# Kernel tuning notes

Measured on AMD Instinct MI355X. Metric: run time of the kernel, lower is better.

## Reference

```python
import jax, jax.numpy as jnp
import numpy as np

B, C, T, V = 8, 64, 16, 207
H, WSZ = 8, 4
EPS = 1e-5


def setup_inputs() -> dict:
    key = jax.random.key(0)
    ks = jax.random.split(key, 16)
    def w(k, shape):
        return jax.random.normal(k, shape, jnp.float32) * 0.02
    inp = {"x": jax.random.normal(ks[0], (B, C, T, V), jnp.float32)}
    for i, s in enumerate("ab"):
        o = 1 + i * 4
        inp[f"qkv_w_{s}"] = w(ks[o], (C, 3 * C))
        inp[f"qkv_b_{s}"] = jnp.zeros((3 * C,), jnp.float32)
        inp[f"proj_w_{s}"] = w(ks[o + 1], (C, C))
        inp[f"proj_b_{s}"] = jnp.zeros((C,), jnp.float32)
        inp[f"ffn_w1_{s}"] = w(ks[o + 2], (C, 4 * C))
        inp[f"ffn_b1_{s}"] = jnp.zeros((4 * C,), jnp.float32)
        inp[f"ffn_w2_{s}"] = w(ks[o + 3], (4 * C, C))
        inp[f"ffn_b2_{s}"] = jnp.zeros((C,), jnp.float32)
        inp[f"ln_{s}1_g"] = jnp.ones((C, T, V), jnp.float32)
        inp[f"ln_{s}1_b"] = jnp.zeros((C, T, V), jnp.float32)
        inp[f"ln_{s}2_g"] = jnp.ones((C, T, V), jnp.float32)
        inp[f"ln_{s}2_b"] = jnp.zeros((C, T, V), jnp.float32)
    inp["n_head"] = H
    inp["window_size"] = WSZ
    return inp


def _layer_norm(x, g, b):
    # LayerNorm over (C, T, V) dims of [B, C, T, V]
    mu = jnp.mean(x, axis=(1, 2, 3), keepdims=True)
    var = jnp.var(x, axis=(1, 2, 3), keepdims=True)
    return (x - mu) / jnp.sqrt(var + EPS) * g + b


def _window_att(x, wqkv, bqkv, wo, bo, n_head, wsz):
    # Joint spatio-temporal attention within windows of `wsz` timesteps.
    b_, c_, t_, v_ = x.shape
    nw = t_ // wsz
    dh = c_ // n_head
    # [B,C,T,V] -> [B,T,V,C] -> [B,nW, wsz*V, C]
    xt = jnp.transpose(x, (0, 2, 3, 1)).reshape(b_, nw, wsz * v_, c_)
    qkv = xt @ wqkv + bqkv  # [B,nW,N,3C]
    q, k, v = jnp.split(qkv, 3, axis=-1)
    def heads(t):
        return t.reshape(b_, nw, -1, n_head, dh).transpose(0, 1, 3, 2, 4)  # [B,nW,H,N,dh]
    q, k, v = heads(q), heads(k), heads(v)
    scale = 1.0 / jnp.sqrt(jnp.asarray(dh, jnp.float32))
    att = jax.nn.softmax(jnp.einsum('bwhnd,bwhmd->bwhnm', q, k) * scale, axis=-1)
    out = jnp.einsum('bwhnm,bwhmd->bwhnd', att, v)
    out = out.transpose(0, 1, 3, 2, 4).reshape(b_, nw, wsz * v_, c_) @ wo + bo
    return out.reshape(b_, t_, v_, c_).transpose(0, 3, 1, 2)


def _ffn(x, w1, b1, w2, b2):
    h = jax.nn.relu(jnp.einsum('bctv,cd->bdtv', x, w1) + b1[None, :, None, None])
    return jnp.einsum('bdtv,dc->bctv', h, w2) + b2[None, :, None, None]


def _block(x, wqkv, bqkv, wo, bo, w1, b1, w2, b2, g1, be1, g2, be2, n_head, wsz):
    x = _window_att(x, wqkv, bqkv, wo, bo, n_head, wsz) + x
    x = _layer_norm(x, g1, be1)
    x = _ffn(x, w1, b1, w2, b2) + x
    x = _layer_norm(x, g2, be2)
    # cyclic shift along time by shift_pixel = wsz // 2
    return jnp.roll(x, -(wsz // 2), axis=2)


def reference(x, qkv_w_a, qkv_b_a, proj_w_a, proj_b_a, ffn_w1_a, ffn_b1_a, ffn_w2_a, ffn_b2_a,
              ln_a1_g, ln_a1_b, ln_a2_g, ln_a2_b,
              qkv_w_b, qkv_b_b, proj_w_b, proj_b_b, ffn_w1_b, ffn_b1_b, ffn_w2_b, ffn_b2_b,
              ln_b1_g, ln_b1_b, ln_b2_g, ln_b2_b, n_head, window_size):
    x = _block(x, qkv_w_a, qkv_b_a, proj_w_a, proj_b_a, ffn_w1_a, ffn_b1_a, ffn_w2_a, ffn_b2_a,
               ln_a1_g, ln_a1_b, ln_a2_g, ln_a2_b, n_head, window_size)
    x = _block(x, qkv_w_b, qkv_b_b, proj_w_b, proj_b_b, ffn_w1_b, ffn_b1_b, ffn_w2_b, ffn_b2_b,
               ln_b1_g, ln_b1_b, ln_b2_g, ln_b2_b, n_head, window_size)
    return x
```

## Files before the change

kernel.cpp:

```cpp
#include <hip/hip_runtime.h>
#include <hip/hip_bf16.h>

#define Bb  8
#define Cc  64
#define Tt  16
#define Vv  207
#define Hh  8
#define DH  8
#define NW  4
#define WSZ 4
#define Nn  (WSZ*Vv)
#define NP  832
#define TV  (Tt*Vv)
#define CTV (Cc*Tt*Vv)
#define S   (Bb*CTV)
#define NBWH (Bb*NW*Hh)
#define EPSF 1e-5f
#define QSCALE 0.51006971401146f
#define FRAG_BWH (52*64*4)
#define LAYER_WSZ 49152

typedef __attribute__((ext_vector_type(4))) short bf16x4;
typedef __attribute__((ext_vector_type(4))) float f32x4;
typedef __attribute__((ext_vector_type(2))) unsigned int u32x2;
typedef __attribute__((ext_vector_type(4))) unsigned int u32x4;

static __device__ __forceinline__ short f2bf(float f) {
    union { float f; unsigned u; } v; v.f = f;
    unsigned r = (v.u + 0x7FFFu + ((v.u >> 16) & 1u)) >> 16;
    return (short)r;
}

static __device__ __forceinline__ bf16x4 pack4(float a, float b, float c, float d) {
    unsigned ua = __builtin_bit_cast(unsigned, a) + 0x8000u;
    unsigned ub = __builtin_bit_cast(unsigned, b) + 0x8000u;
    unsigned uc = __builtin_bit_cast(unsigned, c) + 0x8000u;
    unsigned ud = __builtin_bit_cast(unsigned, d) + 0x8000u;
    u32x2 t;
    t[0] = (ua >> 16) | (ub & 0xFFFF0000u);
    t[1] = (uc >> 16) | (ud & 0xFFFF0000u);
    return __builtin_bit_cast(bf16x4, t);
}

__global__ void prep_kernel(const float* __restrict__ qa, const float* __restrict__ pa,
                            const float* __restrict__ w1a, const float* __restrict__ w2a,
                            const float* __restrict__ qbw, const float* __restrict__ pbw,
                            const float* __restrict__ w1b, const float* __restrict__ w2b,
                            short* __restrict__ wf, float* __restrict__ stats,
                            short* __restrict__ qf, short* __restrict__ kf,
                            short* __restrict__ vf) {
    int i0 = blockIdx.x*256 + threadIdx.x;
    if (i0 < 64) stats[i0] = 0.f;
    for (int i = i0; i < 24576; i += 416*256) {
        int l = i / 12288; int f = i % 12288;
        const float* qw = l ? qbw : qa;
        const float* pw = l ? pbw : pa;
        const float* w1 = l ? w1b : w1a;
        const float* w2 = l ? w2b : w2a;
        short* dst = wf + l*LAYER_WSZ;
        bf16x4 out;
        if (f < 3072) {
            int s = f; int nt = s>>8; int kc = (s>>6)&3; int ln = s&63;
            int li = ln&15; int q = ln>>4;
            #pragma unroll
            for (int j = 0; j < 4; ++j) out[j] = f2bf(qw[(kc*16+q*4+j)*192 + nt*16+li]);
            *((bf16x4*)&dst[s*4]) = out;
        } else if (f < 4096) {
            int s = f-3072; int nt = s>>8; int kc = (s>>6)&3; int ln = s&63;
            int li = ln&15; int q = ln>>4;
            #pragma unroll
            for (int j = 0; j < 4; ++j) out[j] = f2bf(pw[(kc*16+q*4+j)*64 + nt*16+li]);
            *((bf16x4*)&dst[12288 + s*4]) = out;
        } else if (f < 8192) {
            int s = f-4096; int nt = s>>8; int kc = (s>>6)&3; int ln = s&63;
            int li = ln&15; int q = ln>>4;
            #pragma unroll
            for (int j = 0; j < 4; ++j) out[j] = f2bf(w1[(kc*16+q*4+j)*256 + nt*16+li]);
            *((bf16x4*)&dst[16384 + s*4]) = out;
        } else {
            int s = f-8192; int nt = s>>8; int ct = (s>>6)&3; int ln = s&63;
            int li = ln&15; int q = ln>>4;
            #pragma unroll
            for (int j = 0; j < 4; ++j) out[j] = f2bf(w2[(nt*16+q*4+j)*64 + ct*16+li]);
            *((bf16x4*)&dst[32768 + s*4]) = out;
        }
    }
    for (int i = i0; i < NBWH*1664; i += 416*256) {
        int bwh = i / 1664; int rest = i % 1664;
        int nt = rest >> 5; int u = rest & 31;
        size_t base = (size_t)bwh*FRAG_BWH + nt*256;
        *((u32x2*)&qf[base + (32+u)*4]) = (u32x2){0u,0u};
        *((u32x2*)&kf[base + (32+u)*4]) = (u32x2){0u,0u};
        int vlane = (u>>3)*16 + 8 + (u&7);
        short v = ((u&7) == 0) ? (short)0x3F80 : (short)0;
        bf16x4 vv4 = {v,v,v,v};
        *((bf16x4*)&vf[base + vlane*4]) = vv4;
    }
}

__global__ __launch_bounds__(256) void qkv_kernel(const float* __restrict__ src,
        const float* __restrict__ st, const float* __restrict__ g, const float* __restrict__ be,
        const short* __restrict__ wfq, const float* __restrict__ bias,
        short* __restrict__ qf, short* __restrict__ kf, short* __restrict__ vf) {
    __shared__ short wqs[12288];
    __shared__ float bqs[192];
    __shared__ short os[64*196];
    int tid = threadIdx.x;
    int b = blockIdx.x / 52;
    int r0 = (blockIdx.x % 52) * 64;
    const float* xb = src + (size_t)b*CTV;
    {
        const u32x2* wsrc = (const u32x2*)wfq;
        u32x2* wdst = (u32x2*)wqs;
        for (int s = tid; s < 3072; s += 256) wdst[s] = wsrc[s];
    }
    if (tid < 192) bqs[tid] = bias[tid];
    __syncthreads();

    int lane = tid & 63; int wv = tid >> 6;
    int l15 = lane & 15; int quad = lane >> 4;
    int r = r0 + wv*16 + l15;
    int rc = (r < TV) ? r : TV-1;
    int t = rc / Vv; int vv = rc - t*Vv;
    float mean = 0.f, rstd = 0.f; int off;
    if (st) {
        mean = st[b*2] * (1.0f/CTV);
        float var = st[b*2+1] * (1.0f/CTV) - mean*mean;
        rstd = rsqrtf(var + EPSF);
        off = ((t+2)&15)*Vv + vv;
    } else off = rc;

    bf16x4 xf[4];
    #pragma unroll
    for (int kc = 0; kc < 4; ++kc) {
        #pragma unroll
        for (int j = 0; j < 4; ++j) {
            int idx = (kc*16 + quad*4 + j)*TV + off;
            float xv = xb[idx];
            if (st) xv = (xv - mean)*rstd*g[idx] + be[idx];
            xf[kc][j] = f2bf(xv);
        }
    }

    f32x4 accv[12];
    #pragma unroll
    for (int nt = 0; nt < 12; ++nt) {
        float4 bb = *((const float4*)&bqs[nt*16 + quad*4]);
        f32x4 acc = {bb.x, bb.y, bb.z, bb.w};
        #pragma unroll
        for (int kc = 0; kc < 4; ++kc) {
            bf16x4 wf2 = *((const bf16x4*)&wqs[((nt*4 + kc)*64 + lane)*4]);
            acc = __builtin_amdgcn_mfma_f32_16x16x16bf16_1k(wf2, xf[kc], acc, 0, 0, 0);
        }
        accv[nt] = acc;
    }

    int pos = wv*16 + l15;
    #pragma unroll
    for (int nt = 0; nt < 12; ++nt) {
        f32x4 a = accv[nt];
        bf16x4 pk = (nt < 4) ? pack4(a[0]*QSCALE, a[1]*QSCALE, a[2]*QSCALE, a[3]*QSCALE)
                             : pack4(a[0], a[1], a[2], a[3]);
        *((bf16x4*)&os[pos*196 + nt*16 + quad*4]) = pk;
    }
    __syncthreads();

    int pp = tid & 63;
    int rr = r0 + pp;
    bool pv = rr < TV;
    int rrc = pv ? rr : TV-1;
    int t4 = rrc / Vv; int vv4 = rrc - t4*Vv;
    int n2 = (t4 & 3)*Vv + vv4;
    int nt2 = n2 >> 4; int l15n = n2 & 15;
    int quadn = (n2 & 15) >> 2; int jn = n2 & 3;
    int wbase = (b*NW + (t4 >> 2))*Hh;
    if (pv) {
        #pragma unroll
        for (int i = 0; i < 2; ++i) {
            int h = i*4 + wv;
            size_t fb = ((size_t)(wbase+h)*52 + nt2)*256;
            bf16x4 q0 = *((const bf16x4*)&os[pp*196 + h*8]);
            bf16x4 q1 = *((const bf16x4*)&os[pp*196 + h*8 + 4]);
            *((bf16x4*)&qf[fb + l15n*4])        = q0;
            *((bf16x4*)&qf[fb + (16 + l15n)*4]) = q1;
            bf16x4 k0 = *((const bf16x4*)&os[pp*196 + 64 + h*8]);
            bf16x4 k1 = *((const bf16x4*)&os[pp*196 + 64 + h*8 + 4]);
            *((bf16x4*)&kf[fb + l15n*4])        = k0;
            *((bf16x4*)&kf[fb + (16 + l15n)*4]) = k1;
        }
        #pragma unroll
        for (int i = 0; i < 16; ++i) {
            int hd = i*4 + wv;
            int h = hd >> 3; int d = hd & 7;
            vf[(((size_t)(wbase+h)*52 + nt2)*64 + quadn*16 + d)*4 + jn]
                = os[pp*196 + 128 + hd];
        }
    }
}

__global__ __launch_bounds__(1024) void attn_kernel(const short* __restrict__ qf,
        const short* __restrict__ kf, const short* __restrict__ vf,
        short* __restrict__ att) {
    __shared__ short ks2[FRAG_BWH];
    __shared__ short vs2[FRAG_BWH];
    int bwh = blockIdx.x;
    int tid = threadIdx.x;
    int lane = tid & 63;
    int wv = tid >> 6;
    int quad = lane >> 4;
    int l15 = lane & 15;

    {
        const u32x4* kg = (const u32x4*)(kf + (size_t)bwh*FRAG_BWH);
        const u32x4* vg = (const u32x4*)(vf + (size_t)bwh*FRAG_BWH);
        u32x4* kd = (u32x4*)ks2; u32x4* vd = (u32x4*)vs2;
        for (int idx = tid; idx < 1664; idx += 1024) { kd[idx] = kg[idx]; vd[idx] = vg[idx]; }
    }
    __syncthreads();

    int nm = (wv < 4) ? 4 : 3;
    const short* qbase = qf + (size_t)bwh*FRAG_BWH;
    bf16x4 aq[4];
    f32x4 oacc[4];
    #pragma unroll
    for (int i = 0; i < 4; ++i) {
        aq[i] = (bf16x4){0,0,0,0};
        oacc[i] = (f32x4){0.f,0.f,0.f,0.f};
        if (i < nm)
            aq[i] = *(const bf16x4*)(qbase + ((wv + 16*i)*256 + lane*4));
    }

    for (int nt = 0; nt < 52; ++nt) {
        bf16x4 ak = *(const bf16x4*)&ks2[nt*256 + lane*4];
        bf16x4 av = *(const bf16x4*)&vs2[nt*256 + lane*4];
        bool mask = (nt == 51) && (quad == 3);
        #pragma unroll
        for (int i = 0; i < 4; ++i) {
            if (i < nm) {
                f32x4 s = __builtin_amdgcn_mfma_f32_16x16x16bf16_1k(
                              ak, aq[i], (f32x4){0.f,0.f,0.f,0.f}, 0, 0, 0);
                bf16x4 pb = pack4(__builtin_amdgcn_exp2f(s[0]), __builtin_amdgcn_exp2f(s[1]),
                                  __builtin_amdgcn_exp2f(s[2]), __builtin_amdgcn_exp2f(s[3]));
                if (mask) pb = (bf16x4){0,0,0,0};
                oacc[i] = __builtin_amdgcn_mfma_f32_16x16x16bf16_1k(av, pb, oacc[i], 0, 0, 0);
            }
        }
    }
    int h = bwh & 7; int bw = bwh >> 3;
    #pragma unroll
    for (int i = 0; i < 4; ++i) {
        if (i < nm) {
            float ls = __shfl(oacc[i][0], 32 + l15, 64);
            float inv = 1.f / ls;
            int m = (wv + 16*i)*16 + l15;
            if (quad < 2 && m < Nn) {
                bf16x4 ov = pack4(oacc[i][0]*inv, oacc[i][1]*inv,
                                  oacc[i][2]*inv, oacc[i][3]*inv);
                *((bf16x4*)&att[((size_t)bw*Nn + m)*Cc + h*DH + quad*4]) = ov;
            }
        }
    }
}

__global__ __launch_bounds__(256) void proj_kernel(const short* __restrict__ att,
        const short* __restrict__ wfp, const float* __restrict__ bo,
        const float* __restrict__ resid,
        const float* __restrict__ st, const float* __restrict__ g, const float* __restrict__ be,
        float* __restrict__ out, float* __restrict__ stats) {
    __shared__ short wos[4096];
    __shared__ float bos[64];
    __shared__ float r1[256], r2[256];
    int tid = threadIdx.x;
    int b = blockIdx.x / 52;
    int r0 = (blockIdx.x % 52) * 64;
    const float* xb = resid + (size_t)b*CTV;
    {
        const u32x2* wsrc = (const u32x2*)wfp;
        u32x2* wdst = (u32x2*)wos;
        for (int s = tid; s < 1024; s += 256) wdst[s] = wsrc[s];
    }
    if (tid < 64) bos[tid] = bo[tid];
    __syncthreads();

    int lane = tid & 63; int wv = tid >> 6;
    int l15 = lane & 15; int quad = lane >> 4;
    int r = r0 + wv*16 + l15;
    bool valid = r < TV;
    int rc = valid ? r : TV-1;
    int t = rc / Vv; int vv = rc - t*Vv;
    int n = (t & 3)*Vv + vv;
    int bw = b*NW + (t >> 2);
    const short* arow = att + ((size_t)bw*Nn + n)*Cc;
    bf16x4 af[4];
    #pragma unroll
    for (int kc = 0; kc < 4; ++kc)
        af[kc] = *((const bf16x4*)&arow[kc*16 + quad*4]);

    f32x4 acc[4];
    #pragma unroll
    for (int nt = 0; nt < 4; ++nt) {
        float4 bb = *((const float4*)&bos[nt*16 + quad*4]);
        acc[nt] = (f32x4){bb.x, bb.y, bb.z, bb.w};
        #pragma unroll
        for (int kc = 0; kc < 4; ++kc) {
            bf16x4 wf2 = *((const bf16x4*)&wos[((nt*4 + kc)*64 + lane)*4]);
            acc[nt] = __builtin_amdgcn_mfma_f32_16x16x16bf16_1k(wf2, af[kc], acc[nt], 0, 0, 0);
        }
    }
    float mean = 0.f, rstd = 0.f; int off;
    if (st) {
        mean = st[b*2] * (1.0f/CTV);
        float var = st[b*2+1] * (1.0f/CTV) - mean*mean;
        rstd = rsqrtf(var + EPSF);
        off = ((t+2)&15)*Vv + vv;
    } else off = rc;
    float s1 = 0.f, s2 = 0.f;
    if (valid) {
        #pragma unroll
        for (int nt = 0; nt < 4; ++nt) {
            #pragma unroll
            for (int j = 0; j < 4; ++j) {
                int c_out = nt*16 + quad*4 + j;
                int ridx = c_out*TV + off;
                float xv = xb[ridx];
                if (st) xv = (xv - mean)*rstd*g[ridx] + be[ridx];
                float val = acc[nt][j] + xv;
                out[(size_t)b*CTV + (size_t)c_out*TV + r] = val;
                s1 += val; s2 += val*val;
            }
        }
    }
    r1[tid] = s1; r2[tid] = s2;
    __syncthreads();
    for (int o = 128; o > 0; o >>= 1) {
        if (tid < o) { r1[tid] += r1[tid+o]; r2[tid] += r2[tid+o]; }
        __syncthreads();
    }
    if (tid == 0) { atomicAdd(&stats[b*2], r1[0]); atomicAdd(&stats[b*2+1], r2[0]); }
}

__global__ void ln_apply_kernel(const float* __restrict__ x,
                                const float* __restrict__ g,
                                const float* __restrict__ be,
                                const float* __restrict__ stats,
                                float* __restrict__ out,
                                int shift) {
    int idx = blockIdx.x*256 + threadIdx.x;
    if (idx >= S) return;
    int b = idx / CTV; int r = idx % CTV;
    int c = r / TV; int q2 = r % TV; int t = q2 / Vv; int vv = q2 % Vv;
    float mean = stats[b*2] * (1.0f/CTV);
    float var  = stats[b*2+1] * (1.0f/CTV) - mean*mean;
    float rstd = rsqrtf(var + EPSF);
    float val = (x[idx]-mean)*rstd*g[r] + be[r];
    int tout = (t - shift + Tt) % Tt;
    size_t oidx = ((size_t)(b*Cc + c)*Tt + tout)*Vv + vv;
    out[oidx] = val;
}

__global__ __launch_bounds__(256) void ffn_kernel(const float* __restrict__ xin,
        const float* __restrict__ st, const float* __restrict__ g, const float* __restrict__ be,
        const short* __restrict__ wf1, const float* __restrict__ b1,
        const short* __restrict__ wf2g, const float* __restrict__ b2,
        float* __restrict__ out, float* __restrict__ stats) {
    __shared__ short w1s[16384];
    __shared__ short w2s[16384];
    __shared__ short xsf[4096];
    __shared__ float b1s[256];
    __shared__ float b2s[64];
    __shared__ float r1s[256], r2s[256];
    int tid = threadIdx.x;
    int b = blockIdx.x / 52;
    int r0 = (blockIdx.x % 52) * 64;
    const float* xb = xin + (size_t)b*CTV;
    float mean = st[b*2] * (1.0f/CTV);
    float var  = st[b*2+1] * (1.0f/CTV) - mean*mean;
    float rstd = rsqrtf(var + EPSF);

    {
        const u32x2* s1p = (const u32x2*)wf1;
        const u32x2* s2p = (const u32x2*)wf2g;
        u32x2* d1 = (u32x2*)w1s; u32x2* d2 = (u32x2*)w2s;
        for (int s = tid; s < 4096; s += 256) { d1[s] = s1p[s]; d2[s] = s2p[s]; }
    }
    for (int s2 = tid; s2 < 1024; s2 += 256) {
        int wv2 = s2 >> 8; int kc = (s2 >> 6) & 3; int ln = s2 & 63;
        int l15 = ln & 15; int quad = ln >> 4;
        int r = r0 + wv2*16 + l15; if (r >= TV) r = TV-1;
        bf16x4 f;
        #pragma unroll
        for (int j = 0; j < 4; ++j) {
            int idx = (kc*16 + quad*4 + j)*TV + r;
            f[j] = f2bf((xb[idx] - mean)*rstd*g[idx] + be[idx]);
        }
        *((bf16x4*)&xsf[s2*4]) = f;
    }
    b1s[tid] = b1[tid];
    if (tid < 64) b2s[tid] = b2[tid];
    __syncthreads();

    int lane = tid & 63; int wv = tid >> 6;
    int l15 = lane & 15; int quad = lane >> 4;
    bf16x4 xf[4];
    #pragma unroll
    for (int kc = 0; kc < 4; ++kc)
        xf[kc] = *((const bf16x4*)&xsf[((wv*4 + kc)*64 + lane)*4]);

    f32x4 oacc[4];
    #pragma unroll
    for (int ct = 0; ct < 4; ++ct) oacc[ct] = (f32x4){0.f,0.f,0.f,0.f};

    for (int nt = 0; nt < 16; ++nt) {
        float4 bb = *((const float4*)&b1s[nt*16 + quad*4]);
        f32x4 acc = {bb.x, bb.y, bb.z, bb.w};
        #pragma unroll
        for (int kc = 0; kc < 4; ++kc) {
            bf16x4 wfv = *((const bf16x4*)&w1s[((nt*4 + kc)*64 + lane)*4]);
            acc = __builtin_amdgcn_mfma_f32_16x16x16bf16_1k(wfv, xf[kc], acc, 0, 0, 0);
        }
        bf16x4 pf = pack4(fmaxf(acc[0], 0.f), fmaxf(acc[1], 0.f),
                          fmaxf(acc[2], 0.f), fmaxf(acc[3], 0.f));
        #pragma unroll
        for (int ct = 0; ct < 4; ++ct) {
            bf16x4 wfv2 = *((const bf16x4*)&w2s[((nt*4 + ct)*64 + lane)*4]);
            oacc[ct] = __builtin_amdgcn_mfma_f32_16x16x16bf16_1k(wfv2, pf, oacc[ct], 0, 0, 0);
        }
    }
    int r = r0 + wv*16 + l15;
    float s1 = 0.f, s2v = 0.f;
    if (r < TV) {
        #pragma unroll
        for (int ct = 0; ct < 4; ++ct) {
            #pragma unroll
            for (int j = 0; j < 4; ++j) {
                int c_out = ct*16 + quad*4 + j;
                int idx = c_out*TV + r;
                float xv = (xb[idx] - mean)*rstd*g[idx] + be[idx];
                float val = oacc[ct][j] + b2s[c_out] + xv;
                out[(size_t)b*CTV + idx] = val;
                s1 += val; s2v += val*val;
            }
        }
    }
    r1s[tid] = s1; r2s[tid] = s2v;
    __syncthreads();
    for (int o = 128; o > 0; o >>= 1) {
        if (tid < o) { r1s[tid] += r1s[tid+o]; r2s[tid] += r2s[tid+o]; }
        __syncthreads();
    }
    if (tid == 0) { atomicAdd(&stats[b*2], r1s[0]); atomicAdd(&stats[b*2+1], r2s[0]); }
}

extern "C" void kernel_launch(void* const* d_in, const int* in_sizes, int n_in,
                              void* d_out, int out_size, void* d_ws, size_t ws_size,
                              hipStream_t stream) {
    const float* xin = (const float*)d_in[0];

    float* bufA  = (float*)d_ws;
    float* bufB  = bufA + S;
    float* stats = bufB + S;
    short* qf    = (short*)(stats + 64);
    short* kf    = qf + (size_t)NBWH*FRAG_BWH;
    short* vf    = kf + (size_t)NBWH*FRAG_BWH;
    short* att   = vf + (size_t)NBWH*FRAG_BWH;
    short* wf    = att + (size_t)32*Nn*64;

    const float* A0  = (const float*)d_in[1];
    const float* A1  = (const float*)d_in[2];
    const float* A2  = (const float*)d_in[3];
    const float* A3  = (const float*)d_in[4];
    const float* A4  = (const float*)d_in[5];
    const float* A5  = (const float*)d_in[6];
    const float* A6  = (const float*)d_in[7];
    const float* A7  = (const float*)d_in[8];
    const float* A8  = (const float*)d_in[9];
    const float* A9  = (const float*)d_in[10];
    const float* A10 = (const float*)d_in[11];
    const float* A11 = (const float*)d_in[12];
    const float* B0  = (const float*)d_in[13];
    const float* B1  = (const float*)d_in[14];
    const float* B2  = (const float*)d_in[15];
    const float* B3  = (const float*)d_in[16];
    const float* B4  = (const float*)d_in[17];
    const float* B5  = (const float*)d_in[18];
    const float* B6  = (const float*)d_in[19];
    const float* B7  = (const float*)d_in[20];
    const float* B8  = (const float*)d_in[21];
    const float* B9  = (const float*)d_in[22];
    const float* B10 = (const float*)d_in[23];
    const float* B11 = (const float*)d_in[24];

    float* st1a = stats + 0;
    float* st2a = stats + 16;
    float* st1b = stats + 32;
    float* st2b = stats + 48;

    short* wfA = wf;
    short* wfB = wf + LAYER_WSZ;

    prep_kernel<<<416, 256, 0, stream>>>(A0, A2, A4, A6, B0, B2, B4, B6,
                                         wf, stats, qf, kf, vf);

    qkv_kernel<<<Bb*52, 256, 0, stream>>>(xin, nullptr, nullptr, nullptr,
                                          wfA, A1, qf, kf, vf);
    attn_kernel<<<NBWH, 1024, 0, stream>>>(qf, kf, vf, att);
    proj_kernel<<<Bb*52, 256, 0, stream>>>(att, wfA + 12288, A3, xin,
                                           nullptr, nullptr, nullptr, bufB, st1a);
    ffn_kernel<<<Bb*52, 256, 0, stream>>>(bufB, st1a, A8, A9,
                                          wfA + 16384, A5, wfA + 32768, A7, bufB, st2a);
    qkv_kernel<<<Bb*52, 256, 0, stream>>>(bufB, st2a, A10, A11,
                                          wfB, B1, qf, kf, vf);
    attn_kernel<<<NBWH, 1024, 0, stream>>>(qf, kf, vf, att);
    proj_kernel<<<Bb*52, 256, 0, stream>>>(att, wfB + 12288, B3, bufB,
                                           st2a, A10, A11, bufA, st1b);
    ffn_kernel<<<Bb*52, 256, 0, stream>>>(bufA, st1b, B8, B9,
                                          wfB + 16384, B5, wfB + 32768, B7, bufA, st2b);
    ln_apply_kernel<<<(S+255)/256, 256, 0, stream>>>(bufA, B10, B11, st2b, (float*)d_out, WSZ/2);
}
```

Measured before the change: 295.4 us.

## Fuse all stages into one cooperative persistent kernel with grid syncs

Replaces ten separate kernel launches with one cooperative mega-kernel of 512 blocks that runs each stage in turn, separated by grid-wide barriers, with the stages sharing one union of shared-memory layouts. The weight-prep kernel is removed and each block now converts fp32 weights to bf16 MFMA fragments itself when it loads them. Attention is split into two blocks of 256 threads per (batch, window, head) instead of one block of 1024. The aim is to cut launch overhead and inter-kernel gaps. In exchange, every block repeats the weight conversion, grid syncs have their own cost, and blocks 416 to 511 sit idle in most stages.

Measured after the change: 773.6 us. 2.62x slower.

```diff
diff --git a/kernel.cpp b/kernel.cpp
--- a/kernel.cpp
+++ b/kernel.cpp
@@ -1,5 +1,8 @@
 #include <hip/hip_runtime.h>
 #include <hip/hip_bf16.h>
+#include <hip/hip_cooperative_groups.h>
+
+namespace cg = cooperative_groups;
 
 #define Bb  8
 #define Cc  64
@@ -10,7 +13,6 @@
 #define NW  4
 #define WSZ 4
 #define Nn  (WSZ*Vv)
-#define NP  832
 #define TV  (Tt*Vv)
 #define CTV (Cc*Tt*Vv)
 #define S   (Bb*CTV)
@@ -18,7 +20,10 @@
 #define EPSF 1e-5f
 #define QSCALE 0.51006971401146f
 #define FRAG_BWH (52*64*4)
-#define LAYER_WSZ 49152
+
+#define GRID    512
+#define ACTIVE  416
+#define GSTRIDE (GRID*256)
 
 typedef __attribute__((ext_vector_type(4))) short bf16x4;
 typedef __attribute__((ext_vector_type(4))) float f32x4;
@@ -42,50 +47,19 @@
     return __builtin_bit_cast(bf16x4, t);
 }
 
-__global__ void prep_kernel(const float* __restrict__ qa, const float* __restrict__ pa,
-                            const float* __restrict__ w1a, const float* __restrict__ w2a,
-                            const float* __restrict__ qbw, const float* __restrict__ pbw,
-                            const float* __restrict__ w1b, const float* __restrict__ w2b,
-                            short* __restrict__ wf, float* __restrict__ stats,
-                            short* __restrict__ qf, short* __restrict__ kf,
-                            short* __restrict__ vf) {
-    int i0 = blockIdx.x*256 + threadIdx.x;
-    if (i0 < 64) stats[i0] = 0.f;
-    for (int i = i0; i < 24576; i += 416*256) {
-        int l = i / 12288; int f = i % 12288;
-        const float* qw = l ? qbw : qa;
-        const float* pw = l ? pbw : pa;
-        const float* w1 = l ? w1b : w1a;
-        const float* w2 = l ? w2b : w2a;
-        short* dst = wf + l*LAYER_WSZ;
-        bf16x4 out;
-        if (f < 3072) {
-            int s = f; int nt = s>>8; int kc = (s>>6)&3; int ln = s&63;
-            int li = ln&15; int q = ln>>4;
-            #pragma unroll
-            for (int j = 0; j < 4; ++j) out[j] = f2bf(qw[(kc*16+q*4+j)*192 + nt*16+li]);
-            *((bf16x4*)&dst[s*4]) = out;
-        } else if (f < 4096) {
-            int s = f-3072; int nt = s>>8; int kc = (s>>6)&3; int ln = s&63;
-            int li = ln&15; int q = ln>>4;
-            #pragma unroll
-            for (int j = 0; j < 4; ++j) out[j] = f2bf(pw[(kc*16+q*4+j)*64 + nt*16+li]);
-            *((bf16x4*)&dst[12288 + s*4]) = out;
-        } else if (f < 8192) {
-            int s = f-4096; int nt = s>>8; int kc = (s>>6)&3; int ln = s&63;
-            int li = ln&15; int q = ln>>4;
-            #pragma unroll
-            for (int j = 0; j < 4; ++j) out[j] = f2bf(w1[(kc*16+q*4+j)*256 + nt*16+li]);
-            *((bf16x4*)&dst[16384 + s*4]) = out;
-        } else {
-            int s = f-8192; int nt = s>>8; int ct = (s>>6)&3; int ln = s&63;
-            int li = ln&15; int q = ln>>4;
-            #pragma unroll
-            for (int j = 0; j < 4; ++j) out[j] = f2bf(w2[(nt*16+q*4+j)*64 + ct*16+li]);
-            *((bf16x4*)&dst[32768 + s*4]) = out;
-        }
-    }
-    for (int i = i0; i < NBWH*1664; i += 416*256) {
+struct SmQkv { short wqs[12288]; float bqs[192]; short os[64*196]; };
+struct SmAttn { short ks2[FRAG_BWH]; short vs2[FRAG_BWH]; };
+struct SmProj { short wos[4096]; float bos[64]; float r1[256]; float r2[256]; };
+struct SmFfn { short w1s[16384]; short w2s[16384]; short xsf[4096];
+               float b1s[256]; float b2s[64]; float r1s[256]; float r2s[256]; };
+
+static_assert(sizeof(SmQkv) <= sizeof(SmFfn), "");
+static_assert(sizeof(SmAttn) <= sizeof(SmFfn), "");
+static_assert(sizeof(SmProj) <= sizeof(SmFfn), "");
+
+static __device__ void pad_stage(short* __restrict__ qf, short* __restrict__ kf,
+                                 short* __restrict__ vf, int bid, int tid) {
+    for (int i = bid*256 + tid; i < NBWH*1664; i += GSTRIDE) {
         int bwh = i / 1664; int rest = i % 1664;
         int nt = rest >> 5; int u = rest & 31;
         size_t base = (size_t)bwh*FRAG_BWH + nt*256;
@@ -98,23 +72,23 @@
     }
 }
 
-__global__ __launch_bounds__(256) void qkv_kernel(const float* __restrict__ src,
+static __device__ void qkv_stage(const float* __restrict__ src,
         const float* __restrict__ st, const float* __restrict__ g, const float* __restrict__ be,
-        const short* __restrict__ wfq, const float* __restrict__ bias,
-        short* __restrict__ qf, short* __restrict__ kf, short* __restrict__ vf) {
-    __shared__ short wqs[12288];
-    __shared__ float bqs[192];
-    __shared__ short os[64*196];
-    int tid = threadIdx.x;
-    int b = blockIdx.x / 52;
-    int r0 = (blockIdx.x % 52) * 64;
+        const float* __restrict__ qw, const float* __restrict__ bias,
+        short* __restrict__ qf, short* __restrict__ kf, short* __restrict__ vf,
+        int bid, int tid, SmQkv& sm) {
+    int b = bid / 52;
+    int r0 = (bid % 52) * 64;
     const float* xb = src + (size_t)b*CTV;
-    {
-        const u32x2* wsrc = (const u32x2*)wfq;
-        u32x2* wdst = (u32x2*)wqs;
-        for (int s = tid; s < 3072; s += 256) wdst[s] = wsrc[s];
-    }
-    if (tid < 192) bqs[tid] = bias[tid];
+    for (int fs = tid; fs < 3072; fs += 256) {
+        int nt = fs >> 8; int kc = (fs >> 6) & 3; int ln = fs & 63;
+        int li = ln & 15; int q = ln >> 4;
+        bf16x4 o;
+        #pragma unroll
+        for (int j = 0; j < 4; ++j) o[j] = f2bf(qw[(kc*16 + q*4 + j)*192 + nt*16 + li]);
+        *((bf16x4*)&sm.wqs[fs*4]) = o;
+    }
+    if (tid < 192) sm.bqs[tid] = bias[tid];
     __syncthreads();
 
     int lane = tid & 63; int wv = tid >> 6;
@@ -145,11 +119,11 @@
     f32x4 accv[12];
     #pragma unroll
     for (int nt = 0; nt < 12; ++nt) {
-        float4 bb = *((const float4*)&bqs[nt*16 + quad*4]);
+        float4 bb = *((const float4*)&sm.bqs[nt*16 + quad*4]);
         f32x4 acc = {bb.x, bb.y, bb.z, bb.w};
         #pragma unroll
         for (int kc = 0; kc < 4; ++kc) {
-            bf16x4 wf2 = *((const bf16x4*)&wqs[((nt*4 + kc)*64 + lane)*4]);
+            bf16x4 wf2 = *((const bf16x4*)&sm.wqs[((nt*4 + kc)*64 + lane)*4]);
             acc = __builtin_amdgcn_mfma_f32_16x16x16bf16_1k(wf2, xf[kc], acc, 0, 0, 0);
         }
         accv[nt] = acc;
@@ -161,7 +135,7 @@
         f32x4 a = accv[nt];
         bf16x4 pk = (nt < 4) ? pack4(a[0]*QSCALE, a[1]*QSCALE, a[2]*QSCALE, a[3]*QSCALE)
                              : pack4(a[0], a[1], a[2], a[3]);
-        *((bf16x4*)&os[pos*196 + nt*16 + quad*4]) = pk;
+        *((bf16x4*)&sm.os[pos*196 + nt*16 + quad*4]) = pk;
     }
     __syncthreads();
 
@@ -179,12 +153,12 @@
         for (int i = 0; i < 2; ++i) {
             int h = i*4 + wv;
             size_t fb = ((size_t)(wbase+h)*52 + nt2)*256;
-            bf16x4 q0 = *((const bf16x4*)&os[pp*196 + h*8]);
-            bf16x4 q1 = *((const bf16x4*)&os[pp*196 + h*8 + 4]);
+            bf16x4 q0 = *((const bf16x4*)&sm.os[pp*196 + h*8]);
+            bf16x4 q1 = *((const bf16x4*)&sm.os[pp*196 + h*8 + 4]);
             *((bf16x4*)&qf[fb + l15n*4])        = q0;
             *((bf16x4*)&qf[fb + (16 + l15n)*4]) = q1;
-            bf16x4 k0 = *((const bf16x4*)&os[pp*196 + 64 + h*8]);
-            bf16x4 k1 = *((const bf16x4*)&os[pp*196 + 64 + h*8 + 4]);
+            bf16x4 k0 = *((const bf16x4*)&sm.os[pp*196 + 64 + h*8]);
+            bf16x4 k1 = *((const bf16x4*)&sm.os[pp*196 + 64 + h*8 + 4]);
             *((bf16x4*)&kf[fb + l15n*4])        = k0;
             *((bf16x4*)&kf[fb + (16 + l15n)*4]) = k1;
         }
@@ -193,50 +167,46 @@
             int hd = i*4 + wv;
             int h = hd >> 3; int d = hd & 7;
             vf[(((size_t)(wbase+h)*52 + nt2)*64 + quadn*16 + d)*4 + jn]
-                = os[pp*196 + 128 + hd];
-        }
-    }
-}
-
-__global__ __launch_bounds__(1024) void attn_kernel(const short* __restrict__ qf,
-        const short* __restrict__ kf, const short* __restrict__ vf,
-        short* __restrict__ att) {
-    __shared__ short ks2[FRAG_BWH];
-    __shared__ short vs2[FRAG_BWH];
-    int bwh = blockIdx.x;
-    int tid = threadIdx.x;
-    int lane = tid & 63;
-    int wv = tid >> 6;
-    int quad = lane >> 4;
-    int l15 = lane & 15;
-
+                = sm.os[pp*196 + 128 + hd];
+        }
+    }
+}
+
+static __device__ void attn_stage(const short* __restrict__ qf, const short* __restrict__ kf,
+        const short* __restrict__ vf, short* __restrict__ att,
+        int bid, int tid, SmAttn& sm) {
+    int bwh = bid >> 1;
+    int t0 = (bid & 1) * 26;
     {
         const u32x4* kg = (const u32x4*)(kf + (size_t)bwh*FRAG_BWH);
         const u32x4* vg = (const u32x4*)(vf + (size_t)bwh*FRAG_BWH);
-        u32x4* kd = (u32x4*)ks2; u32x4* vd = (u32x4*)vs2;
-        for (int idx = tid; idx < 1664; idx += 1024) { kd[idx] = kg[idx]; vd[idx] = vg[idx]; }
-    }
-    __syncthreads();
-
-    int nm = (wv < 4) ? 4 : 3;
+        u32x4* kd = (u32x4*)sm.ks2; u32x4* vd = (u32x4*)sm.vs2;
+        for (int idx = tid; idx < 1664; idx += 256) { kd[idx] = kg[idx]; vd[idx] = vg[idx]; }
+    }
+    __syncthreads();
+
+    int lane = tid & 63; int wv = tid >> 6;
+    int quad = lane >> 4; int l15 = lane & 15;
+    int ni = (wv < 2) ? 7 : 6;
     const short* qbase = qf + (size_t)bwh*FRAG_BWH;
-    bf16x4 aq[4];
-    f32x4 oacc[4];
-    #pragma unroll
-    for (int i = 0; i < 4; ++i) {
+    bf16x4 aq[7];
+    f32x4 oacc[7];
+    #pragma unroll
+    for (int i = 0; i < 7; ++i) {
         aq[i] = (bf16x4){0,0,0,0};
         oacc[i] = (f32x4){0.f,0.f,0.f,0.f};
-        if (i < nm)
-            aq[i] = *(const bf16x4*)(qbase + ((wv + 16*i)*256 + lane*4));
-    }
-
+        if (i < ni)
+            aq[i] = *(const bf16x4*)(qbase + (size_t)(t0 + wv + 4*i)*256 + lane*4);
+    }
+
+    #pragma unroll 1
     for (int nt = 0; nt < 52; ++nt) {
-        bf16x4 ak = *(const bf16x4*)&ks2[nt*256 + lane*4];
-        bf16x4 av = *(const bf16x4*)&vs2[nt*256 + lane*4];
+        bf16x4 ak = *(const bf16x4*)&sm.ks2[nt*256 + lane*4];
+        bf16x4 av = *(const bf16x4*)&sm.vs2[nt*256 + lane*4];
         bool mask = (nt == 51) && (quad == 3);
         #pragma unroll
-        for (int i = 0; i < 4; ++i) {
-            if (i < nm) {
+        for (int i = 0; i < 7; ++i) {
+            if (i < ni) {
                 f32x4 s = __builtin_amdgcn_mfma_f32_16x16x16bf16_1k(
                               ak, aq[i], (f32x4){0.f,0.f,0.f,0.f}, 0, 0, 0);
                 bf16x4 pb = pack4(__builtin_amdgcn_exp2f(s[0]), __builtin_amdgcn_exp2f(s[1]),
@@ -248,11 +218,11 @@
     }
     int h = bwh & 7; int bw = bwh >> 3;
     #pragma unroll
-    for (int i = 0; i < 4; ++i) {
-        if (i < nm) {
+    for (int i = 0; i < 7; ++i) {
+        if (i < ni) {
             float ls = __shfl(oacc[i][0], 32 + l15, 64);
             float inv = 1.f / ls;
-            int m = (wv + 16*i)*16 + l15;
+            int m = (t0 + wv + 4*i)*16 + l15;
             if (quad < 2 && m < Nn) {
                 bf16x4 ov = pack4(oacc[i][0]*inv, oacc[i][1]*inv,
                                   oacc[i][2]*inv, oacc[i][3]*inv);
@@ -262,24 +232,24 @@
     }
 }
 
-__global__ __launch_bounds__(256) void proj_kernel(const short* __restrict__ att,
-        const short* __restrict__ wfp, const float* __restrict__ bo,
+static __device__ void proj_stage(const short* __restrict__ att,
+        const float* __restrict__ pw, const float* __restrict__ bo,
         const float* __restrict__ resid,
         const float* __restrict__ st, const float* __restrict__ g, const float* __restrict__ be,
-        float* __restrict__ out, float* __restrict__ stats) {
-    __shared__ short wos[4096];
-    __shared__ float bos[64];
-    __shared__ float r1[256], r2[256];
-    int tid = threadIdx.x;
-    int b = blockIdx.x / 52;
-    int r0 = (blockIdx.x % 52) * 64;
+        float* __restrict__ out, float* __restrict__ stats,
+        int bid, int tid, SmProj& sm) {
+    int b = bid / 52;
+    int r0 = (bid % 52) * 64;
     const float* xb = resid + (size_t)b*CTV;
-    {
-        const u32x2* wsrc = (const u32x2*)wfp;
-        u32x2* wdst = (u32x2*)wos;
-        for (int s = tid; s < 1024; s += 256) wdst[s] = wsrc[s];
-    }
-    if (tid < 64) bos[tid] = bo[tid];
+    for (int fs = tid; fs < 1024; fs += 256) {
+        int nt = fs >> 8; int kc = (fs >> 6) & 3; int ln = fs & 63;
+        int li = ln & 15; int q = ln >> 4;
+        bf16x4 o;
+        #pragma unroll
+        for (int j = 0; j < 4; ++j) o[j] = f2bf(pw[(kc*16 + q*4 + j)*64 + nt*16 + li]);
+        *((bf16x4*)&sm.wos[fs*4]) = o;
+    }
+    if (tid < 64) sm.bos[tid] = bo[tid];
     __syncthreads();
 
     int lane = tid & 63; int wv = tid >> 6;
@@ -299,11 +269,11 @@
     f32x4 acc[4];
     #pragma unroll
     for (int nt = 0; nt < 4; ++nt) {
-        float4 bb = *((const float4*)&bos[nt*16 + quad*4]);
+        float4 bb = *((const float4*)&sm.bos[nt*16 + quad*4]);
         acc[nt] = (f32x4){bb.x, bb.y, bb.z, bb.w};
         #pragma unroll
         for (int kc = 0; kc < 4; ++kc) {
-            bf16x4 wf2 = *((const bf16x4*)&wos[((nt*4 + kc)*64 + lane)*4]);
+            bf16x4 wf2 = *((const bf16x4*)&sm.wos[((nt*4 + kc)*64 + lane)*4]);
             acc[nt] = __builtin_amdgcn_mfma_f32_16x16x16bf16_1k(wf2, af[kc], acc[nt], 0, 0, 0);
         }
     }
@@ -330,58 +300,39 @@
             }
         }
     }
-    r1[tid] = s1; r2[tid] = s2;
+    sm.r1[tid] = s1; sm.r2[tid] = s2;
     __syncthreads();
     for (int o = 128; o > 0; o >>= 1) {
-        if (tid < o) { r1[tid] += r1[tid+o]; r2[tid] += r2[tid+o]; }
+        if (tid < o) { sm.r1[tid] += sm.r1[tid+o]; sm.r2[tid] += sm.r2[tid+o]; }
         __syncthreads();
     }
-    if (tid == 0) { atomicAdd(&stats[b*2], r1[0]); atomicAdd(&stats[b*2+1], r2[0]); }
-}
-
-__global__ void ln_apply_kernel(const float* __restrict__ x,
-                                const float* __restrict__ g,
-                                const float* __restrict__ be,
-                                const float* __restrict__ stats,
-                                float* __restrict__ out,
-                                int shift) {
-    int idx = blockIdx.x*256 + threadIdx.x;
-    if (idx >= S) return;
-    int b = idx / CTV; int r = idx % CTV;
-    int c = r / TV; int q2 = r % TV; int t = q2 / Vv; int vv = q2 % Vv;
-    float mean = stats[b*2] * (1.0f/CTV);
-    float var  = stats[b*2+1] * (1.0f/CTV) - mean*mean;
-    float rstd = rsqrtf(var + EPSF);
-    float val = (x[idx]-mean)*rstd*g[r] + be[r];
-    int tout = (t - shift + Tt) % Tt;
-    size_t oidx = ((size_t)(b*Cc + c)*Tt + tout)*Vv + vv;
-    out[oidx] = val;
-}
-
-__global__ __launch_bounds__(256) void ffn_kernel(const float* __restrict__ xin,
+    if (tid == 0) { atomicAdd(&stats[b*2], sm.r1[0]); atomicAdd(&stats[b*2+1], sm.r2[0]); }
+}
+
+static __device__ void ffn_stage(const float* __restrict__ xin,
         const float* __restrict__ st, const float* __restrict__ g, const float* __restrict__ be,
-        const short* __restrict__ wf1, const float* __restrict__ b1,
-        const short* __restrict__ wf2g, const float* __restrict__ b2,
-        float* __restrict__ out, float* __restrict__ stats) {
-    __shared__ short w1s[16384];
-    __shared__ short w2s[16384];
-    __shared__ short xsf[4096];
-    __shared__ float b1s[256];
-    __shared__ float b2s[64];
-    __shared__ float r1s[256], r2s[256];
-    int tid = threadIdx.x;
-    int b = blockIdx.x / 52;
-    int r0 = (blockIdx.x % 52) * 64;
+        const float* __restrict__ w1r, const float* __restrict__ b1,
+        const float* __restrict__ w2r, const float* __restrict__ b2,
+        float* __restrict__ out, float* __restrict__ stats,
+        int bid, int tid, SmFfn& sm) {
+    int b = bid / 52;
+    int r0 = (bid % 52) * 64;
     const float* xb = xin + (size_t)b*CTV;
     float mean = st[b*2] * (1.0f/CTV);
     float var  = st[b*2+1] * (1.0f/CTV) - mean*mean;
     float rstd = rsqrtf(var + EPSF);
 
-    {
-        const u32x2* s1p = (const u32x2*)wf1;
-        const u32x2* s2p = (const u32x2*)wf2g;
-        u32x2* d1 = (u32x2*)w1s; u32x2* d2 = (u32x2*)w2s;
-        for (int s = tid; s < 4096; s += 256) { d1[s] = s1p[s]; d2[s] = s2p[s]; }
+    for (int fs = tid; fs < 4096; fs += 256) {
+        int nt = fs >> 8; int kc = (fs >> 6) & 3; int ln = fs & 63;
+        int li = ln & 15; int q = ln >> 4;
+        bf16x4 o1;
+        #pragma unroll
+        for (int j = 0; j < 4; ++j) o1[j] = f2bf(w1r[(kc*16 + q*4 + j)*256 + nt*16 + li]);
+        *((bf16x4*)&sm.w1s[fs*4]) = o1;
+        bf16x4 o2;
+        #pragma unroll
+        for (int j = 0; j < 4; ++j) o2[j] = f2bf(w2r[(nt*16 + q*4 + j)*64 + kc*16 + li]);
+        *((bf16x4*)&sm.w2s[fs*4]) = o2;
     }
     for (int s2 = tid; s2 < 1024; s2 += 256) {
         int wv2 = s2 >> 8; int kc = (s2 >> 6) & 3; int ln = s2 & 63;
@@ -393,10 +344,10 @@
             int idx = (kc*16 + quad*4 + j)*TV + r;
             f[j] = f2bf((xb[idx] - mean)*rstd*g[idx] + be[idx]);
         }
-        *((bf16x4*)&xsf[s2*4]) = f;
-    }
-    b1s[tid] = b1[tid];
-    if (tid < 64) b2s[tid] = b2[tid];
+        *((bf16x4*)&sm.xsf[s2*4]) = f;
+    }
+    sm.b1s[tid] = b1[tid];
+    if (tid < 64) sm.b2s[tid] = b2[tid];
     __syncthreads();
 
     int lane = tid & 63; int wv = tid >> 6;
@@ -404,25 +355,25 @@
     bf16x4 xf[4];
     #pragma unroll
     for (int kc = 0; kc < 4; ++kc)
-        xf[kc] = *((const bf16x4*)&xsf[((wv*4 + kc)*64 + lane)*4]);
+        xf[kc] = *((const bf16x4*)&sm.xsf[((wv*4 + kc)*64 + lane)*4]);
 
     f32x4 oacc[4];
     #pragma unroll
     for (int ct = 0; ct < 4; ++ct) oacc[ct] = (f32x4){0.f,0.f,0.f,0.f};
 
     for (int nt = 0; nt < 16; ++nt) {
-        float4 bb = *((const float4*)&b1s[nt*16 + quad*4]);
+        float4 bb = *((const float4*)&sm.b1s[nt*16 + quad*4]);
         f32x4 acc = {bb.x, bb.y, bb.z, bb.w};
         #pragma unroll
         for (int kc = 0; kc < 4; ++kc) {
-            bf16x4 wfv = *((const bf16x4*)&w1s[((nt*4 + kc)*64 + lane)*4]);
+            bf16x4 wfv = *((const bf16x4*)&sm.w1s[((nt*4 + kc)*64 + lane)*4]);
             acc = __builtin_amdgcn_mfma_f32_16x16x16bf16_1k(wfv, xf[kc], acc, 0, 0, 0);
         }
         bf16x4 pf = pack4(fmaxf(acc[0], 0.f), fmaxf(acc[1], 0.f),
                           fmaxf(acc[2], 0.f), fmaxf(acc[3], 0.f));
         #pragma unroll
         for (int ct = 0; ct < 4; ++ct) {
-            bf16x4 wfv2 = *((const bf16x4*)&w2s[((nt*4 + ct)*64 + lane)*4]);
+            bf16x4 wfv2 = *((const bf16x4*)&sm.w2s[((nt*4 + ct)*64 + lane)*4]);
             oacc[ct] = __builtin_amdgcn_mfma_f32_16x16x16bf16_1k(wfv2, pf, oacc[ct], 0, 0, 0);
         }
     }
@@ -436,25 +387,90 @@
                 int c_out = ct*16 + quad*4 + j;
                 int idx = c_out*TV + r;
                 float xv = (xb[idx] - mean)*rstd*g[idx] + be[idx];
-                float val = oacc[ct][j] + b2s[c_out] + xv;
+                float val = oacc[ct][j] + sm.b2s[c_out] + xv;
                 out[(size_t)b*CTV + idx] = val;
                 s1 += val; s2v += val*val;
             }
         }
     }
-    r1s[tid] = s1; r2s[tid] = s2v;
+    sm.r1s[tid] = s1; sm.r2s[tid] = s2v;
     __syncthreads();
     for (int o = 128; o > 0; o >>= 1) {
-        if (tid < o) { r1s[tid] += r1s[tid+o]; r2s[tid] += r2s[tid+o]; }
+        if (tid < o) { sm.r1s[tid] += sm.r1s[tid+o]; sm.r2s[tid] += sm.r2s[tid+o]; }
         __syncthreads();
     }
-    if (tid == 0) { atomicAdd(&stats[b*2], r1s[0]); atomicAdd(&stats[b*2+1], r2s[0]); }
+    if (tid == 0) { atomicAdd(&stats[b*2], sm.r1s[0]); atomicAdd(&stats[b*2+1], sm.r2s[0]); }
+}
+
+static __device__ void ln_stage(const float* __restrict__ x,
+                                const float* __restrict__ g,
+                                const float* __restrict__ be,
+                                const float* __restrict__ stats,
+                                float* __restrict__ out, int bid, int tid) {
+    for (int idx = bid*256 + tid; idx < S; idx += GSTRIDE) {
+        int b = idx / CTV; int r = idx % CTV;
+        int c = r / TV; int q2 = r % TV; int t = q2 / Vv; int vv = q2 % Vv;
+        float mean = stats[b*2] * (1.0f/CTV);
+        float var  = stats[b*2+1] * (1.0f/CTV) - mean*mean;
+        float rstd = rsqrtf(var + EPSF);
+        float val = (x[idx]-mean)*rstd*g[r] + be[r];
+        int tout = (t - 2 + Tt) & 15;
+        size_t oidx = ((size_t)(b*Cc + c)*Tt + tout)*Vv + vv;
+        out[oidx] = val;
+    }
+}
+
+struct MegaArgs {
+    const float* xin;
+    const float *A0,*A1,*A2,*A3,*A4,*A5,*A6,*A7,*A8,*A9,*A10,*A11;
+    const float *B0,*B1,*B2,*B3,*B4,*B5,*B6,*B7,*B8,*B9,*B10,*B11;
+    float* out;
+    float* bufA; float* bufB; float* stats;
+    short* qf; short* kf; short* vf; short* att;
+};
+
+__global__ void __launch_bounds__(256, 2) mega_kernel(MegaArgs a) {
+    __shared__ __align__(16) char smraw[sizeof(SmFfn)];
+    cg::grid_group grid = cg::this_grid();
+    int bid = blockIdx.x, tid = threadIdx.x;
+
+    pad_stage(a.qf, a.kf, a.vf, bid, tid);
+    if (bid == 0 && tid < 64) a.stats[tid] = 0.f;
+    if (bid < ACTIVE)
+        qkv_stage(a.xin, nullptr, nullptr, nullptr, a.A0, a.A1,
+                  a.qf, a.kf, a.vf, bid, tid, *(SmQkv*)smraw);
+    grid.sync();
+    attn_stage(a.qf, a.kf, a.vf, a.att, bid, tid, *(SmAttn*)smraw);
+    grid.sync();
+    if (bid < ACTIVE)
+        proj_stage(a.att, a.A2, a.A3, a.xin, nullptr, nullptr, nullptr,
+                   a.bufB, a.stats + 0, bid, tid, *(SmProj*)smraw);
+    grid.sync();
+    if (bid < ACTIVE)
+        ffn_stage(a.bufB, a.stats + 0, a.A8, a.A9, a.A4, a.A5, a.A6, a.A7,
+                  a.bufB, a.stats + 16, bid, tid, *(SmFfn*)smraw);
+    grid.sync();
+    if (bid < ACTIVE)
+        qkv_stage(a.bufB, a.stats + 16, a.A10, a.A11, a.B0, a.B1,
+                  a.qf, a.kf, a.vf, bid, tid, *(SmQkv*)smraw);
+    grid.sync();
+    attn_stage(a.qf, a.kf, a.vf, a.att, bid, tid, *(SmAttn*)smraw);
+    grid.sync();
+    if (bid < ACTIVE)
+        proj_stage(a.att, a.B2, a.B3, a.bufB, a.stats + 16, a.A10, a.A11,
+                   a.bufA, a.stats + 32, bid, tid, *(SmProj*)smraw);
+    grid.sync();
+    if (bid < ACTIVE)
+        ffn_stage(a.bufA, a.stats + 32, a.B8, a.B9, a.B4, a.B5, a.B6, a.B7,
+                  a.bufA, a.stats + 48, bid, tid, *(SmFfn*)smraw);
+    grid.sync();
+    ln_stage(a.bufA, a.B10, a.B11, a.stats + 48, a.out, bid, tid);
 }
 
 extern "C" void kernel_launch(void* const* d_in, const int* in_sizes, int n_in,
                               void* d_out, int out_size, void* d_ws, size_t ws_size,
                               hipStream_t stream) {
-    const float* xin = (const float*)d_in[0];
+    (void)in_sizes; (void)n_in; (void)out_size; (void)ws_size;
 
     float* bufA  = (float*)d_ws;
     float* bufB  = bufA + S;
@@ -463,57 +479,26 @@
     short* kf    = qf + (size_t)NBWH*FRAG_BWH;
     short* vf    = kf + (size_t)NBWH*FRAG_BWH;
     short* att   = vf + (size_t)NBWH*FRAG_BWH;
-    short* wf    = att + (size_t)32*Nn*64;
-
-    const float* A0  = (const float*)d_in[1];
-    const float* A1  = (const float*)d_in[2];
-    const float* A2  = (const float*)d_in[3];
-    const float* A3  = (const float*)d_in[4];
-    const float* A4  = (const float*)d_in[5];
-    const float* A5  = (const float*)d_in[6];
-    const float* A6  = (const float*)d_in[7];
-    const float* A7  = (const float*)d_in[8];
-    const float* A8  = (const float*)d_in[9];
-    const float* A9  = (const float*)d_in[10];
-    const float* A10 = (const float*)d_in[11];
-    const float* A11 = (const float*)d_in[12];
-    const float* B0  = (const float*)d_in[13];
-    const float* B1  = (const float*)d_in[14];
-    const float* B2  = (const float*)d_in[15];
-    const float* B3  = (const float*)d_in[16];
-    const float* B4  = (const float*)d_in[17];
-    const float* B5  = (const float*)d_in[18];
-    const float* B6  = (const float*)d_in[19];
-    const float* B7  = (const float*)d_in[20];
-    const float* B8  = (const float*)d_in[21];
-    const float* B9  = (const float*)d_in[22];
-    const float* B10 = (const float*)d_in[23];
-    const float* B11 = (const float*)d_in[24];
-
-    float* st1a = stats + 0;
-    float* st2a = stats + 16;
-    float* st1b = stats + 32;
-    float* st2b = stats + 48;
-
-    short* wfA = wf;
-    short* wfB = wf + LAYER_WSZ;
-
-    prep_kernel<<<416, 256, 0, stream>>>(A0, A2, A4, A6, B0, B2, B4, B6,
-                                         wf, stats, qf, kf, vf);
-
-    qkv_kernel<<<Bb*52, 256, 0, stream>>>(xin, nullptr, nullptr, nullptr,
-                                          wfA, A1, qf, kf, vf);
-    attn_kernel<<<NBWH, 1024, 0, stream>>>(qf, kf, vf, att);
-    proj_kernel<<<Bb*52, 256, 0, stream>>>(att, wfA + 12288, A3, xin,
-                                           nullptr, nullptr, nullptr, bufB, st1a);
-    ffn_kernel<<<Bb*52, 256, 0, stream>>>(bufB, st1a, A8, A9,
-                                          wfA + 16384, A5, wfA + 32768, A7, bufB, st2a);
-    qkv_kernel<<<Bb*52, 256, 0, stream>>>(bufB, st2a, A10, A11,
-                                          wfB, B1, qf, kf, vf);
-    attn_kernel<<<NBWH, 1024, 0, stream>>>(qf, kf, vf, att);
-    proj_kernel<<<Bb*52, 256, 0, stream>>>(att, wfB + 12288, B3, bufB,
-                                           st2a, A10, A11, bufA, st1b);
-    ffn_kernel<<<Bb*52, 256, 0, stream>>>(bufA, st1b, B8, B9,
-                                          wfB + 16384, B5, wfB + 32768, B7, bufA, st2b);
-    ln_apply_kernel<<<(S+255)/256, 256, 0, stream>>>(bufA, B10, B11, st2b, (float*)d_out, WSZ/2);
-}
+
+    MegaArgs ha;
+    ha.xin = (const float*)d_in[0];
+    ha.A0  = (const float*)d_in[1];  ha.A1  = (const float*)d_in[2];
+    ha.A2  = (const float*)d_in[3];  ha.A3  = (const float*)d_in[4];
+    ha.A4  = (const float*)d_in[5];  ha.A5  = (const float*)d_in[6];
+    ha.A6  = (const float*)d_in[7];  ha.A7  = (const float*)d_in[8];
+    ha.A8  = (const float*)d_in[9];  ha.A9  = (const float*)d_in[10];
+    ha.A10 = (const float*)d_in[11]; ha.A11 = (const float*)d_in[12];
+    ha.B0  = (const float*)d_in[13]; ha.B1  = (const float*)d_in[14];
+    ha.B2  = (const float*)d_in[15]; ha.B3  = (const float*)d_in[16];
+    ha.B4  = (const float*)d_in[17]; ha.B5  = (const float*)d_in[18];
+    ha.B6  = (const float*)d_in[19]; ha.B7  = (const float*)d_in[20];
+    ha.B8  = (const float*)d_in[21]; ha.B9  = (const float*)d_in[22];
+    ha.B10 = (const float*)d_in[23]; ha.B11 = (const float*)d_in[24];
+    ha.out = (float*)d_out;
+    ha.bufA = bufA; ha.bufB = bufB; ha.stats = stats;
+    ha.qf = qf; ha.kf = kf; ha.vf = vf; ha.att = att;
+
+    void* kargs[] = { (void*)&ha };
+    hipLaunchCooperativeKernel(reinterpret_cast<void*>(mega_kernel),
+                               dim3(GRID), dim3(256), kargs, 0, stream);
+}
```
